# Kernel optimization log

Measured on AMD Instinct MI355X. Metric: run time of the kernel, lower is better.

## Reference

```python
import jax, jax.numpy as jnp
import numpy as np

K_NUM = 4      # kernel_num: size of dynamic kernel bank
KS = 3         # spatial kernel size


def _fdconv(x, w_fr, w_fi, b, a1w, a1b, a2w, a2b):
    """Frequency-dynamic conv: kernels parameterized in the Fourier domain,
    mixed per-sample by a GAP->MLP->softmax attention over the kernel bank,
    then applied as a per-sample 3x3 conv (batched via grouped conv).
    x: [B,Cin,H,W]; w_fr/w_fi: [K,Cout,Cin,3,2] (rfft2 coeffs); b: [Cout]."""
    B, Cin, H, W = x.shape
    # per-sample kernel attention
    gap = x.mean((2, 3))                                   # [B,Cin]
    h = jax.nn.relu(gap @ a1w + a1b)                       # [B,hidden]
    attn = jax.nn.softmax(h @ a2w + a2b, axis=-1)          # [B,K]
    # synthesize spatial kernels from frequency coefficients
    w = jnp.fft.irfft2(w_fr + 1j * w_fi, s=(KS, KS), axes=(-2, -1))  # [K,Co,Ci,3,3]
    w = w.astype(x.dtype)
    wd = jnp.einsum('bk,koihw->boihw', attn, w)            # [B,Co,Ci,3,3]
    Co = wd.shape[1]
    # per-sample conv via feature_group_count=B grouped conv
    xg = x.reshape(1, B * Cin, H, W)
    wg = wd.reshape(B * Co, Cin, KS, KS)
    y = jax.lax.conv_general_dilated(
        xg, wg, window_strides=(1, 1), padding='SAME',
        dimension_numbers=('NCHW', 'OIHW', 'NCHW'),
        feature_group_count=B)
    return y.reshape(B, Co, H, W) + b[None, :, None, None]


def setup_inputs() -> dict:
    key = jax.random.key(0)
    ks = jax.random.split(key, 16)
    B, Cin, Cout, H, W = 16, 128, 256, 128, 128
    h1, h2 = Cin // 4, Cout // 4
    FR = KS // 2 + 1  # rfft bins along last dim
    s = 0.05
    return {
        'x': jax.random.normal(ks[0], (B, Cin, H, W), jnp.float32),
        # conv1 (Cin->Cout)
        'w1_fr': jax.random.normal(ks[1], (K_NUM, Cout, Cin, KS, FR), jnp.float32) * s,
        'w1_fi': jax.random.normal(ks[2], (K_NUM, Cout, Cin, KS, FR), jnp.float32) * s,
        'b1': jnp.zeros((Cout,), jnp.float32),
        'a1w1': jax.random.normal(ks[3], (Cin, h1), jnp.float32) * s,
        'a1b1': jnp.zeros((h1,), jnp.float32),
        'a1w2': jax.random.normal(ks[4], (h1, K_NUM), jnp.float32) * s,
        'a1b2': jnp.zeros((K_NUM,), jnp.float32),
        # conv2 (Cout->Cout)
        'w2_fr': jax.random.normal(ks[5], (K_NUM, Cout, Cout, KS, FR), jnp.float32) * s,
        'w2_fi': jax.random.normal(ks[6], (K_NUM, Cout, Cout, KS, FR), jnp.float32) * s,
        'b2': jnp.zeros((Cout,), jnp.float32),
        'a2w1': jax.random.normal(ks[7], (Cout, h2), jnp.float32) * s,
        'a2b1': jnp.zeros((h2,), jnp.float32),
        'a2w2': jax.random.normal(ks[8], (h2, K_NUM), jnp.float32) * s,
        'a2b2': jnp.zeros((K_NUM,), jnp.float32),
    }


def reference(x, w1_fr, w1_fi, b1, a1w1, a1b1, a1w2, a1b2,
              w2_fr, w2_fi, b2, a2w1, a2b1, a2w2, a2b2):
    y = jax.nn.relu(_fdconv(x, w1_fr, w1_fi, b1, a1w1, a1b1, a1w2, a1b2))
    y = jax.nn.relu(_fdconv(y, w2_fr, w2_fi, b2, a2w1, a2b1, a2w2, a2b2))
    return y
```

## Files before the change

kernel.cpp:

```cpp
#include <hip/hip_runtime.h>
#include <hip/hip_bf16.h>
#include <math.h>


#define K_NUM 4
typedef __attribute__((ext_vector_type(8))) short short8;
typedef __attribute__((ext_vector_type(4))) float f32x4;

__device__ inline float bf2f(short s) {
  unsigned u = ((unsigned)(unsigned short)s) << 16;
  return __uint_as_float(u);
}
__device__ inline short f2bf(float f) {
  __hip_bfloat16 h = __float2bfloat16(f);
  return (short)*reinterpret_cast<unsigned short*>(&h);
}

__global__ void fd_gap_kernel(const float* __restrict__ x, float* __restrict__ out, int HW) {
  const float4* p = (const float4*)(x + (size_t)blockIdx.x * HW);
  int n4 = HW >> 2;
  float s = 0.f;
  for (int i = threadIdx.x; i < n4; i += blockDim.x) {
    float4 v = p[i];
    s += v.x + v.y + v.z + v.w;
  }
  for (int off = 32; off > 0; off >>= 1) s += __shfl_down(s, off, 64);
  __shared__ float wsum[4];
  int lane = threadIdx.x & 63, w = threadIdx.x >> 6;
  if (lane == 0) wsum[w] = s;
  __syncthreads();
  if (threadIdx.x == 0) {
    float t = 0.f;
    int nw = blockDim.x >> 6;
    for (int i = 0; i < nw; ++i) t += wsum[i];
    out[blockIdx.x] = t / (float)HW;
  }
}

__global__ __launch_bounds__(1024) void gap_t_part_kernel(
    const short* __restrict__ y, float* __restrict__ part) {
  const int HW = 16384, CO = 256;
  int b = blockIdx.y, ch = blockIdx.x;
  int t = threadIdx.x;
  int tg = t & 31, pg = t >> 5;
  const short* base = y + ((size_t)b * HW + (size_t)ch * 1024) * CO + tg * 8;
  float s[8];
#pragma unroll
  for (int j = 0; j < 8; ++j) s[j] = 0.f;
  for (int px = pg; px < 1024; px += 32) {
    short8 v = *(const short8*)(base + (size_t)px * CO);
#pragma unroll
    for (int j = 0; j < 8; ++j) s[j] += bf2f(v[j]);
  }
  __shared__ float red[32][32][8];
#pragma unroll
  for (int j = 0; j < 8; ++j) red[pg][tg][j] = s[j];
  __syncthreads();
  if (t < 256) {
    float tot = 0.f;
    const float* r = (const float*)red;
#pragma unroll
    for (int p = 0; p < 32; ++p) tot += r[p * 256 + t];
    part[((size_t)b * 16 + ch) * 256 + t] = tot;
  }
}
__global__ void gap_t_reduce_kernel(const float* __restrict__ part, float* __restrict__ gap) {
  int b = blockIdx.x, co = threadIdx.x;
  float s = 0.f;
  for (int c = 0; c < 16; ++c) s += part[(b * 16 + c) * 256 + co];
  gap[b * 256 + co] = s * (1.f / 16384.f);
}

__global__ void fd_attn_kernel(const float* __restrict__ gap, int C, int Hd,
                               const float* __restrict__ w1, const float* __restrict__ b1,
                               const float* __restrict__ w2, const float* __restrict__ b2,
                               float* __restrict__ attn) {
  int b = blockIdx.x, j = threadIdx.x;
  __shared__ float h[64];
  __shared__ float z[K_NUM];
  if (j < Hd) {
    float s = b1[j];
    const float* g = gap + (size_t)b * C;
    for (int c = 0; c < C; ++c) s = fmaf(g[c], w1[c * Hd + j], s);
    h[j] = fmaxf(s, 0.f);
  }
  __syncthreads();
  if (j < K_NUM) {
    float s = b2[j];
    for (int c = 0; c < Hd; ++c) s = fmaf(h[c], w2[c * K_NUM + j], s);
    z[j] = s;
  }
  __syncthreads();
  if (j == 0) {
    float m = z[0];
    for (int k = 1; k < K_NUM; ++k) m = fmaxf(m, z[k]);
    float e[K_NUM], sum = 0.f;
    for (int k = 0; k < K_NUM; ++k) { e[k] = expf(z[k] - m); sum += e[k]; }
    for (int k = 0; k < K_NUM; ++k) attn[b * K_NUM + k] = e[k] / sum;
  }
}

__global__ void fd_synth_t_kernel(const float* __restrict__ wfr, const float* __restrict__ wfi,
                                  const float* __restrict__ attn, short* __restrict__ wdt,
                                  int B, int CO, int CI) {
  size_t gid = (size_t)blockIdx.x * blockDim.x + threadIdx.x;
  size_t total = (size_t)B * CI * CO;
  if (gid >= total) return;
  int ci = (int)(gid % CI);
  size_t t = gid / CI;
  int co = (int)(t % CO);
  int b = (int)(t / CO);

  float a[K_NUM];
  for (int k = 0; k < K_NUM; ++k) a[k] = attn[b * K_NUM + k];

  float Fr[3][2], Fi[3][2];
  for (int u = 0; u < 3; ++u) for (int v = 0; v < 2; ++v) { Fr[u][v] = 0.f; Fi[u][v] = 0.f; }
  for (int k = 0; k < K_NUM; ++k) {
    size_t base = ((((size_t)k * CO + co) * CI + ci) * 3) * 2;
    const float* pr = wfr + base;
    const float* pi = wfi + base;
    float ak = a[k];
    for (int u = 0; u < 3; ++u)
      for (int v = 0; v < 2; ++v) {
        Fr[u][v] = fmaf(ak, pr[u * 2 + v], Fr[u][v]);
        Fi[u][v] = fmaf(ak, pi[u * 2 + v], Fi[u][v]);
      }
  }

  const float CS[3] = {1.f, -0.5f, -0.5f};
  const float SN[3] = {0.f, 0.8660254037844386f, -0.8660254037844386f};
  float outv[9];
  for (int ai = 0; ai < 3; ++ai) {
    float Gr[2], Gi[2];
    for (int v = 0; v < 2; ++v) {
      float gr = 0.f, gi = 0.f;
      for (int u = 0; u < 3; ++u) {
        int idx = (u * ai) % 3;
        gr += Fr[u][v] * CS[idx] - Fi[u][v] * SN[idx];
        gi += Fr[u][v] * SN[idx] + Fi[u][v] * CS[idx];
      }
      Gr[v] = gr * (1.f / 3.f);
      Gi[v] = gi * (1.f / 3.f);
    }
    for (int bi = 0; bi < 3; ++bi)
      outv[ai * 3 + bi] = (Gr[0] + 2.f * (Gr[1] * CS[bi] - Gi[1] * SN[bi])) * (1.f / 3.f);
  }
  int ci8 = ci >> 3, cil = ci & 7;
  for (int s = 0; s < 9; ++s)
    wdt[((((size_t)b * 9 + s) * (CI / 8) + ci8) * CO + co) * 8 + cil] = f2bf(outv[s]);
}

__global__ __launch_bounds__(256) void transpose_bf16_kernel(
    const float* __restrict__ in, short* __restrict__ out, int C) {
  const int HW = 16384;
  __shared__ short t[64 * 40];
  int tid = threadIdx.x;
  int px0 = blockIdx.x * 64, c0 = blockIdx.y * 32, b = blockIdx.z;
  int px = tid & 63, cb = tid >> 6;
#pragma unroll
  for (int i = 0; i < 8; ++i) {
    int c = i * 4 + cb;
    float v = in[((size_t)b * C + c0 + c) * HW + px0 + px];
    t[px * 40 + c] = f2bf(v);
  }
  __syncthreads();
  int px2 = tid >> 2, g = tid & 3;
  short8 v = *(const short8*)(t + px2 * 40 + g * 8);
  *(short8*)(out + ((size_t)b * HW + px0 + px2) * C + c0 + g * 8) = v;
}

template <int CI, int MODE>
__global__ __launch_bounds__(256) void conv_mfma_kernel(
    const short* __restrict__ xin,
    const short* __restrict__ wdt,
    const float* __restrict__ bias,
    short* __restrict__ yout_t,
    float* __restrict__ yout_f) {
  const int H = 128, W = 128, HW = H * W, CO = 256;
  const int NKC = CI / 32;
  __shared__ short xs[18 * 18 * 40];

  const int tid = threadIdx.x;
  const int w = tid >> 6;
  const int lane = tid & 63;
  const int l15 = lane & 15, l4 = lane >> 4;
  const int tx0 = (blockIdx.x & 7) * 16, ty0 = (blockIdx.x >> 3) * 16;
  const int co0 = blockIdx.y * 64;
  const int b = blockIdx.z;

  f32x4 acc[4][4];
#pragma unroll
  for (int i = 0; i < 4; ++i)
#pragma unroll
    for (int j = 0; j < 4; ++j)
      acc[i][j] = (f32x4){0.f, 0.f, 0.f, 0.f};

  for (int kc = 0; kc < NKC; ++kc) {
    __syncthreads();
#pragma unroll
    for (int i = 0; i < 6; ++i) {
      int idx = i * 256 + tid;
      if (idx < 1296) {
        int pxi = idx >> 2, g = idx & 3;
        int r = pxi / 18, c = pxi - r * 18;
        int gy = ty0 + r - 1, gx = tx0 + c - 1;
        short8 v = {0, 0, 0, 0, 0, 0, 0, 0};
        if ((unsigned)gy < (unsigned)H && (unsigned)gx < (unsigned)W)
          v = *(const short8*)(xin + ((size_t)b * HW + gy * W + gx) * CI + kc * 32 + g * 8);
        *(short8*)(xs + pxi * 40 + g * 8) = v;
      }
    }
    __syncthreads();

#pragma unroll
    for (int dc = 0; dc < 3; ++dc) {
      short8 xf[6];
#pragma unroll
      for (int rr = 0; rr < 6; ++rr)
        xf[rr] = *(const short8*)(xs + ((4 * w + rr) * 18 + l15 + dc) * 40 + l4 * 8);
      short8 wf[3][4];
#pragma unroll
      for (int dr = 0; dr < 3; ++dr) {
        const short* wp = wdt + ((((size_t)b * 9 + dr * 3 + dc) * (CI / 8) + kc * 4 + l4) * CO + co0 + l15) * 8;
#pragma unroll
        for (int cf = 0; cf < 4; ++cf)
          wf[dr][cf] = *(const short8*)(wp + cf * 128);
      }
#pragma unroll
      for (int dr = 0; dr < 3; ++dr)
#pragma unroll
        for (int nf = 0; nf < 4; ++nf)
#pragma unroll
          for (int cf = 0; cf < 4; ++cf) {
            if (MODE == 0)
              acc[nf][cf] = __builtin_amdgcn_mfma_f32_16x16x32_bf16(
                  xf[nf + dr], wf[dr][cf], acc[nf][cf], 0, 0, 0);
            else
              acc[nf][cf] = __builtin_amdgcn_mfma_f32_16x16x32_bf16(
                  wf[dr][cf], xf[nf + dr], acc[nf][cf], 0, 0, 0);
          }
    }
  }

  if (MODE == 0) {
#pragma unroll
    for (int cf = 0; cf < 4; ++cf) {
      float bs = bias[co0 + cf * 16 + l15];
#pragma unroll
      for (int nf = 0; nf < 4; ++nf) {
        int row = ty0 + 4 * w + nf;
#pragma unroll
        for (int r = 0; r < 4; ++r) {
          int col = tx0 + l4 * 4 + r;
          float v = fmaxf(acc[nf][cf][r] + bs, 0.f);
          yout_t[((size_t)b * HW + (size_t)row * W + col) * CO + co0 + cf * 16 + l15] = f2bf(v);
        }
      }
    }
  } else {
#pragma unroll
    for (int cf = 0; cf < 4; ++cf) {
#pragma unroll
      for (int r = 0; r < 4; ++r) {
        int co = co0 + cf * 16 + l4 * 4 + r;
        float bs = bias[co];
#pragma unroll
        for (int nf = 0; nf < 4; ++nf) {
          int row = ty0 + 4 * w + nf;
          int col = tx0 + l15;
          yout_f[((size_t)b * CO + co) * HW + (size_t)row * W + col] =
              fmaxf(acc[nf][cf][r] + bs, 0.f);
        }
      }
    }
  }
}

extern "C" void kernel_launch(void* const* d_in, const int* in_sizes, int n_in,
                              void* d_out, int out_size, void* d_ws, size_t ws_size,
                              hipStream_t stream) {
  const int B = 16, CIN = 128, COUT = 256, H = 128, W = 128, HW = H * W;

  const float* x    = (const float*)d_in[0];
  const float* w1fr = (const float*)d_in[1];
  const float* w1fi = (const float*)d_in[2];
  const float* b1   = (const float*)d_in[3];
  const float* a1w1 = (const float*)d_in[4];
  const float* a1b1 = (const float*)d_in[5];
  const float* a1w2 = (const float*)d_in[6];
  const float* a1b2 = (const float*)d_in[7];
  const float* w2fr = (const float*)d_in[8];
  const float* w2fi = (const float*)d_in[9];
  const float* b2   = (const float*)d_in[10];
  const float* a2w1 = (const float*)d_in[11];
  const float* a2b1 = (const float*)d_in[12];
  const float* a2w2 = (const float*)d_in[13];
  const float* a2b2 = (const float*)d_in[14];
  float* outf = (float*)d_out;

  short* xt = (short*)d_out;

  char* wsb = (char*)d_ws;
  short* y1t  = (short*)wsb;
  short* wdt  = (short*)(wsb + 134217728);
  float* gprt = (float*)(wsb + 134217728 + 18874368);
  float* gap  = (float*)(wsb + 134217728 + 18874368 + 262144);
  float* attn = (float*)(wsb + 134217728 + 18874368 + 262144 + 16384);

  transpose_bf16_kernel<<<dim3(HW / 64, CIN / 32, B), 256, 0, stream>>>(x, xt, CIN);
  fd_gap_kernel<<<B * CIN, 256, 0, stream>>>(x, gap, HW);
  fd_attn_kernel<<<B, 64, 0, stream>>>(gap, CIN, CIN / 4, a1w1, a1b1, a1w2, a1b2, attn);
  fd_synth_t_kernel<<<(B * CIN * COUT) / 256, 256, 0, stream>>>(w1fr, w1fi, attn, wdt, B, COUT, CIN);
  conv_mfma_kernel<128, 0><<<dim3(64, 4, 16), 256, 0, stream>>>(xt, wdt, b1, y1t, nullptr);

  gap_t_part_kernel<<<dim3(16, B), 1024, 0, stream>>>(y1t, gprt);
  gap_t_reduce_kernel<<<B, 256, 0, stream>>>(gprt, gap);
  fd_attn_kernel<<<B, 64, 0, stream>>>(gap, COUT, COUT / 4, a2w1, a2b1, a2w2, a2b2, attn);
  fd_synth_t_kernel<<<(B * COUT * COUT) / 256, 256, 0, stream>>>(w2fr, w2fi, attn, wdt, B, COUT, COUT);
  conv_mfma_kernel<256, 1><<<dim3(64, 4, 16), 256, 0, stream>>>(y1t, wdt, b2, nullptr, outf);
}
```

Measured before the change: 1.099 ms.

## Double-buffer conv input tile and widen block to 512 threads covering 128 output channels

The conv kernel now uses two LDS buffers and prefetches the next input-channel chunk into registers while MFMAs run on the current one. This cuts one barrier per iteration and overlaps global loads with compute. Blocks grow to 512 threads (8 waves), with two wave groups each covering 64 output channels. The shared input halo tile is therefore loaded once per 128 channels instead of once per 64, halving redundant input traffic. The cost is twice the LDS, more live registers for the prefetch, and half as many blocks.

Result: faster. 1.042 ms (-5.2%).

```diff
diff --git a/kernel.cpp b/kernel.cpp
--- a/kernel.cpp
+++ b/kernel.cpp
@@ -171,7 +171,7 @@
 }
 
 template <int CI, int MODE>
-__global__ __launch_bounds__(256) void conv_mfma_kernel(
+__global__ __launch_bounds__(512) void conv_mfma_kernel(
     const short* __restrict__ xin,
     const short* __restrict__ wdt,
     const float* __restrict__ bias,
@@ -179,15 +179,50 @@
     float* __restrict__ yout_f) {
   const int H = 128, W = 128, HW = H * W, CO = 256;
   const int NKC = CI / 32;
-  __shared__ short xs[18 * 18 * 40];
+  __shared__ short xs[2][18 * 18 * 40];
 
   const int tid = threadIdx.x;
   const int w = tid >> 6;
+  const int wy = w & 3, wc = w >> 2;
   const int lane = tid & 63;
   const int l15 = lane & 15, l4 = lane >> 4;
   const int tx0 = (blockIdx.x & 7) * 16, ty0 = (blockIdx.x >> 3) * 16;
-  const int co0 = blockIdx.y * 64;
+  const int cob = blockIdx.y * 128 + wc * 64;
   const int b = blockIdx.z;
+
+  int sr[3], sc[3], sg[3];
+#pragma unroll
+  for (int i = 0; i < 3; ++i) {
+    int idx = i * 512 + tid;
+    int pxi = idx >> 2;
+    sg[i] = idx & 3;
+    sr[i] = pxi / 18;
+    sc[i] = pxi - sr[i] * 18;
+  }
+  const bool has2 = (tid < 272);
+
+  short8 pre[3];
+  auto stage_load = [&](int kc) {
+#pragma unroll
+    for (int i = 0; i < 3; ++i) {
+      if (i < 2 || has2) {
+        int gy = ty0 + sr[i] - 1, gx = tx0 + sc[i] - 1;
+        short8 v = {0, 0, 0, 0, 0, 0, 0, 0};
+        if ((unsigned)gy < (unsigned)H && (unsigned)gx < (unsigned)W)
+          v = *(const short8*)(xin + ((size_t)b * HW + gy * W + gx) * CI + kc * 32 + sg[i] * 8);
+        pre[i] = v;
+      }
+    }
+  };
+  auto stage_write = [&](short* buf) {
+#pragma unroll
+    for (int i = 0; i < 3; ++i) {
+      if (i < 2 || has2) {
+        int pxi = sr[i] * 18 + sc[i];
+        *(short8*)(buf + pxi * 40 + sg[i] * 8) = pre[i];
+      }
+    }
+  };
 
   f32x4 acc[4][4];
 #pragma unroll
@@ -196,33 +231,26 @@
     for (int j = 0; j < 4; ++j)
       acc[i][j] = (f32x4){0.f, 0.f, 0.f, 0.f};
 
+  stage_load(0);
+  stage_write(xs[0]);
+  __syncthreads();
+
+  int cur = 0;
   for (int kc = 0; kc < NKC; ++kc) {
-    __syncthreads();
-#pragma unroll
-    for (int i = 0; i < 6; ++i) {
-      int idx = i * 256 + tid;
-      if (idx < 1296) {
-        int pxi = idx >> 2, g = idx & 3;
-        int r = pxi / 18, c = pxi - r * 18;
-        int gy = ty0 + r - 1, gx = tx0 + c - 1;
-        short8 v = {0, 0, 0, 0, 0, 0, 0, 0};
-        if ((unsigned)gy < (unsigned)H && (unsigned)gx < (unsigned)W)
-          v = *(const short8*)(xin + ((size_t)b * HW + gy * W + gx) * CI + kc * 32 + g * 8);
-        *(short8*)(xs + pxi * 40 + g * 8) = v;
-      }
-    }
-    __syncthreads();
+    const bool more = (kc + 1 < NKC);
+    if (more) stage_load(kc + 1);
+    const short* bufc = xs[cur];
 
 #pragma unroll
     for (int dc = 0; dc < 3; ++dc) {
       short8 xf[6];
 #pragma unroll
       for (int rr = 0; rr < 6; ++rr)
-        xf[rr] = *(const short8*)(xs + ((4 * w + rr) * 18 + l15 + dc) * 40 + l4 * 8);
+        xf[rr] = *(const short8*)(bufc + ((4 * wy + rr) * 18 + l15 + dc) * 40 + l4 * 8);
       short8 wf[3][4];
 #pragma unroll
       for (int dr = 0; dr < 3; ++dr) {
-        const short* wp = wdt + ((((size_t)b * 9 + dr * 3 + dc) * (CI / 8) + kc * 4 + l4) * CO + co0 + l15) * 8;
+        const short* wp = wdt + ((((size_t)b * 9 + dr * 3 + dc) * (CI / 8) + kc * 4 + l4) * CO + cob + l15) * 8;
 #pragma unroll
         for (int cf = 0; cf < 4; ++cf)
           wf[dr][cf] = *(const short8*)(wp + cf * 128);
@@ -241,20 +269,24 @@
                   wf[dr][cf], xf[nf + dr], acc[nf][cf], 0, 0, 0);
           }
     }
+
+    if (more) stage_write(xs[cur ^ 1]);
+    __syncthreads();
+    cur ^= 1;
   }
 
   if (MODE == 0) {
 #pragma unroll
     for (int cf = 0; cf < 4; ++cf) {
-      float bs = bias[co0 + cf * 16 + l15];
+      float bs = bias[cob + cf * 16 + l15];
 #pragma unroll
       for (int nf = 0; nf < 4; ++nf) {
-        int row = ty0 + 4 * w + nf;
+        int row = ty0 + 4 * wy + nf;
 #pragma unroll
         for (int r = 0; r < 4; ++r) {
           int col = tx0 + l4 * 4 + r;
           float v = fmaxf(acc[nf][cf][r] + bs, 0.f);
-          yout_t[((size_t)b * HW + (size_t)row * W + col) * CO + co0 + cf * 16 + l15] = f2bf(v);
+          yout_t[((size_t)b * HW + (size_t)row * W + col) * CO + cob + cf * 16 + l15] = f2bf(v);
         }
       }
     }
@@ -263,11 +295,11 @@
     for (int cf = 0; cf < 4; ++cf) {
 #pragma unroll
       for (int r = 0; r < 4; ++r) {
-        int co = co0 + cf * 16 + l4 * 4 + r;
+        int co = cob + cf * 16 + l4 * 4 + r;
         float bs = bias[co];
 #pragma unroll
         for (int nf = 0; nf < 4; ++nf) {
-          int row = ty0 + 4 * w + nf;
+          int row = ty0 + 4 * wy + nf;
           int col = tx0 + l15;
           yout_f[((size_t)b * CO + co) * HW + (size_t)row * W + col] =
               fmaxf(acc[nf][cf][r] + bs, 0.f);
@@ -312,11 +344,11 @@
   fd_gap_kernel<<<B * CIN, 256, 0, stream>>>(x, gap, HW);
   fd_attn_kernel<<<B, 64, 0, stream>>>(gap, CIN, CIN / 4, a1w1, a1b1, a1w2, a1b2, attn);
   fd_synth_t_kernel<<<(B * CIN * COUT) / 256, 256, 0, stream>>>(w1fr, w1fi, attn, wdt, B, COUT, CIN);
-  conv_mfma_kernel<128, 0><<<dim3(64, 4, 16), 256, 0, stream>>>(xt, wdt, b1, y1t, nullptr);
+  conv_mfma_kernel<128, 0><<<dim3(64, 2, 16), 512, 0, stream>>>(xt, wdt, b1, y1t, nullptr);
 
   gap_t_part_kernel<<<dim3(16, B), 1024, 0, stream>>>(y1t, gprt);
   gap_t_reduce_kernel<<<B, 256, 0, stream>>>(gprt, gap);
   fd_attn_kernel<<<B, 64, 0, stream>>>(gap, COUT, COUT / 4, a2w1, a2b1, a2w2, a2b2, attn);
   fd_synth_t_kernel<<<(B * COUT * COUT) / 256, 256, 0, stream>>>(w2fr, w2fi, attn, wdt, B, COUT, COUT);
-  conv_mfma_kernel<256, 1><<<dim3(64, 4, 16), 256, 0, stream>>>(y1t, wdt, b2, nullptr, outf);
-}
+  conv_mfma_kernel<256, 1><<<dim3(64, 2, 16), 512, 0, stream>>>(y1t, wdt, b2, nullptr, outf);
+}
```
